# Performance work log

Measured on AMD Instinct MI355X. Metric: run time of the kernel, lower is better.

## Reference

```python
import jax, jax.numpy as jnp
import numpy as np

N = 8192        # nodes
IN_DIM = 512    # input feature dim
H = 8           # heads (hardcoded as 8 in original forward)
HID = 64        # out_feats per head
T = 10          # top-K threshold from settings['T']
OUT = 3         # classes
NEG = -9e15
NE_HALF = 131072  # half edges; graph made symmetric -> 262144 edges


def setup_inputs() -> dict:
    key = jax.random.key(0)
    ks = jax.random.split(key, 10)
    feat = jax.random.normal(ks[0], (N, IN_DIM), jnp.float32)

    def edges(k):
        k1, k2, k3 = jax.random.split(k, 3)
        u = jax.random.randint(k1, (NE_HALF,), 0, N, jnp.int32)
        v = jax.random.randint(k2, (NE_HALF,), 0, N, jnp.int32)
        src = jnp.concatenate([u, v])
        dst = jnp.concatenate([v, u])
        t = jax.random.uniform(k3, (NE_HALF,), jnp.float32) * 0.1  # TransM values
        trans = jnp.concatenate([t, t])
        return src, dst, trans

    src0, dst0, trans0 = edges(ks[1])
    src1, dst1, trans1 = edges(ks[2])
    fc_w0 = jax.random.normal(ks[3], (IN_DIM, H * HID), jnp.float32) * 0.05
    fc_w1 = jax.random.normal(ks[4], (IN_DIM, H * HID), jnp.float32) * 0.05
    sem_w1 = jax.random.normal(ks[5], (H * HID, 128), jnp.float32) * 0.05
    sem_b1 = jnp.zeros((128,), jnp.float32)
    sem_w2 = jax.random.normal(ks[6], (128,), jnp.float32) * 0.05
    lin_w = jax.random.normal(ks[7], (H * HID, OUT), jnp.float32) * 0.05
    lin_b = jnp.zeros((OUT,), jnp.float32)
    return dict(feat=feat, src0=src0, dst0=dst0, trans0=trans0,
                src1=src1, dst1=dst1, trans1=trans1,
                fc_w0=fc_w0, fc_w1=fc_w1, sem_w1=sem_w1, sem_b1=sem_b1,
                sem_w2=sem_w2, lin_w=lin_w, lin_b=lin_b)


def _rohe_conv(feat, src, dst, trans, fc_w):
    f = (feat @ fc_w).reshape(N, H, HID)               # (N,H,HID) projected feats
    # per-edge per-head dot products (same math as dense matmul + edge gather)
    e = jnp.einsum('ehd,ehd->eh', f[src], f[dst])      # (Ne,H)
    vals = trans * e.sum(-1)                           # (Ne,)  (e * e_trans).sum over heads
    # dense sparse->to_dense attn matrix, duplicates coalesced by sum
    A = jnp.zeros((N, N), f.dtype).at[src, dst].add(vals)
    kth = jax.lax.top_k(A, T)[0][:, -1]                # per-row T-th largest
    thr = jnp.maximum(kth, 0.0)                        # clamp(min=0)
    Am = jnp.where(A < thr[:, None], NEG, A)
    gathered = Am[dst, src]                            # == Am.T[src, dst]
    e = jnp.where((gathered < -100.0)[:, None], NEG, e)
    # edge softmax grouped by destination node, per head
    m = jax.ops.segment_max(e, dst, num_segments=N)
    ex = jnp.exp(e - m[dst])
    s = jax.ops.segment_sum(ex, dst, num_segments=N)
    a = ex / s[dst]                                    # (Ne,H)
    # u_mul_e + sum aggregation
    out = jax.ops.segment_sum(f[src] * a[:, :, None], dst, num_segments=N)
    return jax.nn.elu(out).reshape(N, H * HID)         # activation=F.elu, flatten(1)


def reference(feat, src0, dst0, trans0, src1, dst1, trans1,
              fc_w0, fc_w1, sem_w1, sem_b1, sem_w2, lin_w, lin_b):
    z0 = _rohe_conv(feat, src0, dst0, trans0, fc_w0)
    z1 = _rohe_conv(feat, src1, dst1, trans1, fc_w1)
    z = jnp.stack([z0, z1], axis=1)                    # (N, M=2, D)
    # SemanticAttention: project -> tanh -> score, mean over nodes, softmax over metapaths
    w = jnp.tanh(z @ sem_w1 + sem_b1) @ sem_w2         # (N, M)
    beta = jax.nn.softmax(w.mean(0))                   # (M,)
    h = (z * beta[None, :, None]).sum(1)               # (N, D)
    return h @ lin_w + lin_b                           # final nn.Linear
```

## Files before the change

kernel.cpp:

```cpp
#include <hip/hip_runtime.h>
#include <math.h>

#define NN      8192
#define DIM     512
#define NHEAD   8
#define HID     64
#define NE      262144
#define NE_HALF 131072
#define CMASK   (NE_HALF - 1)
#define TOPK    10
#define NEGV    -9e15f
#define MAXD    160
#define MAXC    64

typedef __attribute__((ext_vector_type(8))) short short8;
typedef __attribute__((ext_vector_type(4))) float f32x4;
typedef __attribute__((ext_vector_type(2))) int i32x2;
typedef __attribute__((ext_vector_type(4))) int i32x4;

__device__ __forceinline__ float bf2f(unsigned int h) {
    return __uint_as_float(h << 16);
}
__device__ __forceinline__ unsigned short f2bf(float x) {
    unsigned int u = __float_as_uint(x);
    unsigned int r = (u + 0x7fff + ((u >> 16) & 1)) >> 16;
    return (unsigned short)r;
}

__device__ __forceinline__ void scatter_body(int j, int c,
                                             const int* __restrict__ src0,
                                             const int* __restrict__ src1,
                                             const int* __restrict__ dst0,
                                             const int* __restrict__ dst1,
                                             const float* __restrict__ trans0,
                                             const float* __restrict__ trans1,
                                             int* curF, int* curC,
                                             i32x2* __restrict__ ed,
                                             i32x4* __restrict__ ce) {
    const int* s = c ? src1 : src0;
    const int* dt = c ? dst1 : dst0;
    int v = s[j];
    int dv = dt[j];
    int p = atomicAdd(&curF[c * NN + v], 1);
    if (p < MAXD) {
        i32x2 pk; pk.x = j; pk.y = dv;
        ed[(size_t)(c * NN + v) * MAXD + p] = pk;
    }
    if (j < NE_HALF) {
        const float* tr = c ? trans1 : trans0;
        int q = atomicAdd(&curC[c * NN + v], 1);
        if (q < MAXC) {
            i32x4 ck;
            ck.x = j; ck.y = dv; ck.z = __float_as_int(tr[j]); ck.w = 0;
            ce[(size_t)(c * NN + v) * MAXC + q] = ck;
        }
    }
}

__device__ __forceinline__ void gemm_body(int b,
                                          const unsigned short* __restrict__ Ah,
                                          const unsigned short* __restrict__ Al,
                                          const unsigned short* __restrict__ Bh,
                                          const unsigned short* __restrict__ Bl,
                                          float* __restrict__ Cf,
                                          unsigned short* __restrict__ Ch) {
    __shared__ unsigned short Ash[128][32];
    __shared__ unsigned short Asl[128][32];
    __shared__ unsigned short Bsh[64][32];
    __shared__ unsigned short Bsl[64][32];
    const int bm = (b >> 3) * 128;
    const int bn = (b & 7) * 64;
    const int tid = threadIdx.x;
    const int lane = tid & 63;
    const int wave = tid >> 6;
    const int wm = (wave >> 1) * 64, wn = (wave & 1) * 32;
    const int fr = lane & 15, fq = lane >> 4;
    const int sr = tid >> 2, sc = (tid & 3) * 8;
    f32x4 acc[4][2] = {};
    const unsigned short* Ahg = Ah + (size_t)(bm + sr) * DIM + sc;
    const unsigned short* Alg = Al + (size_t)(bm + sr) * DIM + sc;
    const unsigned short* Bhg = Bh + (size_t)(bn + sr) * DIM + sc;
    const unsigned short* Blg = Bl + (size_t)(bn + sr) * DIM + sc;
    for (int kb = 0; kb < DIM; kb += 32) {
        __syncthreads();
        __builtin_amdgcn_global_load_lds(
            (const __attribute__((address_space(1))) void*)(Ahg + kb),
            (__attribute__((address_space(3))) void*)(&Ash[sr][sc]), 16, 0, 0);
        __builtin_amdgcn_global_load_lds(
            (const __attribute__((address_space(1))) void*)(Ahg + (size_t)64 * DIM + kb),
            (__attribute__((address_space(3))) void*)(&Ash[sr + 64][sc]), 16, 0, 0);
        __builtin_amdgcn_global_load_lds(
            (const __attribute__((address_space(1))) void*)(Alg + kb),
            (__attribute__((address_space(3))) void*)(&Asl[sr][sc]), 16, 0, 0);
        __builtin_amdgcn_global_load_lds(
            (const __attribute__((address_space(1))) void*)(Alg + (size_t)64 * DIM + kb),
            (__attribute__((address_space(3))) void*)(&Asl[sr + 64][sc]), 16, 0, 0);
        if (sr < 64) {
            __builtin_amdgcn_global_load_lds(
                (const __attribute__((address_space(1))) void*)(Bhg + kb),
                (__attribute__((address_space(3))) void*)(&Bsh[sr][sc]), 16, 0, 0);
            __builtin_amdgcn_global_load_lds(
                (const __attribute__((address_space(1))) void*)(Blg + kb),
                (__attribute__((address_space(3))) void*)(&Bsl[sr][sc]), 16, 0, 0);
        }
        __syncthreads();
        short8 ah[4], al[4], bh[2], bl[2];
        #pragma unroll
        for (int i = 0; i < 4; i++) {
            ah[i] = *(const short8*)&Ash[wm + i * 16 + fr][fq * 8];
            al[i] = *(const short8*)&Asl[wm + i * 16 + fr][fq * 8];
        }
        #pragma unroll
        for (int i = 0; i < 2; i++) {
            bh[i] = *(const short8*)&Bsh[wn + i * 16 + fr][fq * 8];
            bl[i] = *(const short8*)&Bsl[wn + i * 16 + fr][fq * 8];
        }
        #pragma unroll
        for (int mi = 0; mi < 4; mi++)
            #pragma unroll
            for (int ni = 0; ni < 2; ni++) {
                acc[mi][ni] = __builtin_amdgcn_mfma_f32_16x16x32_bf16(ah[mi], bh[ni], acc[mi][ni], 0, 0, 0);
                acc[mi][ni] = __builtin_amdgcn_mfma_f32_16x16x32_bf16(al[mi], bh[ni], acc[mi][ni], 0, 0, 0);
                acc[mi][ni] = __builtin_amdgcn_mfma_f32_16x16x32_bf16(ah[mi], bl[ni], acc[mi][ni], 0, 0, 0);
            }
    }
    #pragma unroll
    for (int mi = 0; mi < 4; mi++)
        #pragma unroll
        for (int ni = 0; ni < 2; ni++)
            #pragma unroll
            for (int r = 0; r < 4; r++) {
                int row = bm + wm + mi * 16 + fq * 4 + r;
                int col = bn + wn + ni * 16 + fr;
                float v = acc[mi][ni][r];
                size_t off = (size_t)row * DIM + col;
                Cf[off] = v;
                Ch[off] = f2bf(v);
            }
}

__device__ __forceinline__ void edge_body(int n,
                                          const float* __restrict__ Cf,
                                          const int* __restrict__ cdeg,
                                          const i32x4* __restrict__ ce,
                                          float* __restrict__ e,
                                          float* __restrict__ vals) {
    int d = cdeg[n];
    if (d > MAXC) d = MAXC;
    if (d <= 0) return;
    int wave = threadIdx.x >> 6, lane = threadIdx.x & 63;
    const float4* pf = (const float4*)(Cf + (size_t)n * DIM);
    float4 f0 = pf[lane * 2], f1 = pf[lane * 2 + 1];
    const size_t s0 = (size_t)n * MAXC;
    for (int base = wave * 4; base < d; base += 16) {
        int em = d - base; if (em > 4) em = 4;
        i32x4 c[4];
        #pragma unroll
        for (int t = 0; t < 4; t++)
            c[t] = ce[s0 + base + (t < em ? t : 0)];
        float4 b0[4], b1[4];
        #pragma unroll
        for (int t = 0; t < 4; t++) {
            const float4* q = (const float4*)(Cf + (size_t)c[t].y * DIM);
            b0[t] = q[lane * 2];
            b1[t] = q[lane * 2 + 1];
        }
        float p[4];
        #pragma unroll
        for (int t = 0; t < 4; t++) {
            p[t]  = f0.x * b0[t].x + f0.y * b0[t].y + f0.z * b0[t].z + f0.w * b0[t].w;
            p[t] += f1.x * b1[t].x + f1.y * b1[t].y + f1.z * b1[t].z + f1.w * b1[t].w;
            p[t] += __shfl_xor(p[t], 1);
            p[t] += __shfl_xor(p[t], 2);
            p[t] += __shfl_xor(p[t], 4);
        }
        if ((lane & 7) == 0) {
            int h = lane >> 3;
            #pragma unroll
            for (int t = 0; t < 4; t++)
                if (t < em) e[(size_t)c[t].x * NHEAD + h] = p[t];
        }
        #pragma unroll
        for (int t = 0; t < 4; t++) {
            p[t] += __shfl_xor(p[t], 8);
            p[t] += __shfl_xor(p[t], 16);
            p[t] += __shfl_xor(p[t], 32);
        }
        if (lane == 0) {
            #pragma unroll
            for (int t = 0; t < 4; t++)
                if (t < em) vals[c[t].x] = __int_as_float(c[t].z) * p[t];
        }
    }
}

__device__ __forceinline__ void conv_body(int blk,
                                          const int* __restrict__ deg,
                                          const i32x2* __restrict__ ed,
                                          const float* __restrict__ e,
                                          const float* __restrict__ vals,
                                          const unsigned short* __restrict__ fb,
                                          unsigned short* __restrict__ zb) {
    const int tid = threadIdx.x;
    const int w = tid >> 6, lane = tid & 63;
    const int n = blk * 4 + w;
    int d = deg[n];
    if (d > MAXD) d = MAXD;
    const size_t s0 = (size_t)n * MAXD;
    __shared__ int   ssrc[4][MAXD];
    __shared__ int   sjc[4][MAXD];
    __shared__ float sval[4][MAXD];
    __shared__ float svc[4][MAXD];
    __shared__ unsigned char lead[4][MAXD];
    __shared__ short sk[4][MAXD];
    __shared__ float sms[4][2][NHEAD];
    __shared__ int nkept[4];

    for (int i = lane; i < d; i += 64) {
        i32x2 pk = ed[s0 + i];
        int jc = pk.x & CMASK;
        sjc[w][i] = jc;
        ssrc[w][i] = pk.y;
        sval[w][i] = vals[jc];
    }
    __syncthreads();
    for (int i = lane; i < d; i += 64) {
        int c = ssrc[w][i];
        float sum = 0.f;
        bool leader = true;
        for (int k = 0; k < d; k++) {
            if (ssrc[w][k] == c) {
                sum += sval[w][k];
                if (k < i) leader = false;
            }
        }
        svc[w][i] = sum;
        lead[w][i] = leader ? 1 : 0;
    }
    __syncthreads();
    {
        float v[3];
        #pragma unroll
        for (int s = 0; s < 3; s++) v[s] = -1.f;
        int cnt = 0;
        #pragma unroll
        for (int s = 0; s < 3; s++) {
            int i = lane + s * 64;
            if (i < d && lead[w][i] && svc[w][i] > 0.f) { v[s] = svc[w][i]; cnt++; }
        }
        cnt += __shfl_xor(cnt, 1);  cnt += __shfl_xor(cnt, 2);
        cnt += __shfl_xor(cnt, 4);  cnt += __shfl_xor(cnt, 8);
        cnt += __shfl_xor(cnt, 16); cnt += __shfl_xor(cnt, 32);
        float thr = 0.f;
        if (cnt >= TOPK) {
            unsigned long long key = 0;
            for (int t = 0; t < TOPK; t++) {
                unsigned int bb = 0; int bs = 0;
                #pragma unroll
                for (int s = 0; s < 3; s++) {
                    if (v[s] > 0.f) {
                        unsigned int b = __float_as_uint(v[s]);
                        if (b > bb) { bb = b; bs = s; }
                    }
                }
                key = ((unsigned long long)bb << 12) | (unsigned)(lane << 3) | (unsigned)bs;
                unsigned long long o;
                o = __shfl_xor(key, 1);  if (o > key) key = o;
                o = __shfl_xor(key, 2);  if (o > key) key = o;
                o = __shfl_xor(key, 4);  if (o > key) key = o;
                o = __shfl_xor(key, 8);  if (o > key) key = o;
                o = __shfl_xor(key, 16); if (o > key) key = o;
                o = __shfl_xor(key, 32); if (o > key) key = o;
                int owner = (int)((key >> 3) & 63);
                if (owner == lane) v[key & 7] = -1.f;
            }
            thr = __uint_as_float((unsigned int)(key >> 12));
        }
        int base = 0;
        for (int s = 0; s * 64 < d; s++) {
            int i = s * 64 + lane;
            bool kp = (i < d) && (svc[w][i] >= thr);
            unsigned long long m = __ballot(kp);
            int pos = base + __popcll(m & ((1ull << lane) - 1ull));
            if (kp) sk[w][pos] = (short)i;
            base += (int)__popcll(m);
        }
        if (base == 0) {
            for (int i = lane; i < d; i += 64) sk[w][i] = (short)i;
            if (lane == 0) nkept[w] = -d;
        } else if (lane == 0) nkept[w] = base;
    }
    __syncthreads();
    int nk = nkept[w];
    bool uni = nk < 0;
    int dk = uni ? -nk : nk;
    if (!uni) {
        int h = lane & 7, sub = lane >> 3;
        float m = -INFINITY;
        for (int k = sub; k < dk; k += 8)
            m = fmaxf(m, e[(size_t)sjc[w][sk[w][k]] * NHEAD + h]);
        m = fmaxf(m, __shfl_xor(m, 8));
        m = fmaxf(m, __shfl_xor(m, 16));
        m = fmaxf(m, __shfl_xor(m, 32));
        float s = 0.f;
        for (int k = sub; k < dk; k += 8)
            s += expf(e[(size_t)sjc[w][sk[w][k]] * NHEAD + h] - m);
        s += __shfl_xor(s, 8);
        s += __shfl_xor(s, 16);
        s += __shfl_xor(s, 32);
        if (sub == 0) { sms[w][0][h] = m; sms[w][1][h] = 1.0f / s; }
    }
    __syncthreads();
    int c0 = lane * 8;
    int h = lane >> 3;
    float a0 = 0.f, a1 = 0.f, a2 = 0.f, a3 = 0.f;
    float a4 = 0.f, a5 = 0.f, a6 = 0.f, a7 = 0.f;
    if (uni) {
        for (int k = 0; k < dk; k++) {
            int ii = sk[w][k];
            uint4 v = *(const uint4*)(fb + (size_t)ssrc[w][ii] * DIM + c0);
            a0 += bf2f(v.x & 0xffffu); a1 += bf2f(v.x >> 16);
            a2 += bf2f(v.y & 0xffffu); a3 += bf2f(v.y >> 16);
            a4 += bf2f(v.z & 0xffffu); a5 += bf2f(v.z >> 16);
            a6 += bf2f(v.w & 0xffffu); a7 += bf2f(v.w >> 16);
        }
        float invd = 1.0f / (float)d;
        a0 *= invd; a1 *= invd; a2 *= invd; a3 *= invd;
        a4 *= invd; a5 *= invd; a6 *= invd; a7 *= invd;
    } else {
        float m_h = sms[w][0][h], is_h = sms[w][1][h];
        for (int kb = 0; kb < dk; kb += 8) {
            int rem = dk - kb; if (rem > 8) rem = 8;
            float wv = 0.f;
            {
                int t = lane & 7;
                if (t < rem) {
                    int ii = sk[w][kb + t];
                    wv = expf(e[(size_t)sjc[w][ii] * NHEAD + h] - m_h) * is_h;
                }
            }
#define AGG(j) { \
            float wgt = __shfl(wv, (lane & 56) | (j)); \
            int ii2 = sk[w][kb + (j)]; \
            uint4 vv = *(const uint4*)(fb + (size_t)ssrc[w][ii2] * DIM + c0); \
            a0 += wgt * bf2f(vv.x & 0xffffu); a1 += wgt * bf2f(vv.x >> 16); \
            a2 += wgt * bf2f(vv.y & 0xffffu); a3 += wgt * bf2f(vv.y >> 16); \
            a4 += wgt * bf2f(vv.z & 0xffffu); a5 += wgt * bf2f(vv.z >> 16); \
            a6 += wgt * bf2f(vv.w & 0xffffu); a7 += wgt * bf2f(vv.w >> 16); }
            if (rem == 8) {
                AGG(0) AGG(1) AGG(2) AGG(3) AGG(4) AGG(5) AGG(6) AGG(7)
            } else {
                for (int j = 0; j < rem; j++) AGG(j)
            }
#undef AGG
        }
    }
    a0 = a0 > 0.f ? a0 : expf(a0) - 1.f;
    a1 = a1 > 0.f ? a1 : expf(a1) - 1.f;
    a2 = a2 > 0.f ? a2 : expf(a2) - 1.f;
    a3 = a3 > 0.f ? a3 : expf(a3) - 1.f;
    a4 = a4 > 0.f ? a4 : expf(a4) - 1.f;
    a5 = a5 > 0.f ? a5 : expf(a5) - 1.f;
    a6 = a6 > 0.f ? a6 : expf(a6) - 1.f;
    a7 = a7 > 0.f ? a7 : expf(a7) - 1.f;
    uint4 o;
    o.x = (unsigned)f2bf(a0) | ((unsigned)f2bf(a1) << 16);
    o.y = (unsigned)f2bf(a2) | ((unsigned)f2bf(a3) << 16);
    o.z = (unsigned)f2bf(a4) | ((unsigned)f2bf(a5) << 16);
    o.w = (unsigned)f2bf(a6) | ((unsigned)f2bf(a7) << 16);
    *(uint4*)(zb + (size_t)n * DIM + c0) = o;
}

__device__ __forceinline__ void lin_body(int blk,
                                         const unsigned short* __restrict__ zb,
                                         const float* __restrict__ lin_w,
                                         float* __restrict__ y) {
    int tid = threadIdx.x;
    int w = tid >> 6, lane = tid & 63;
    int n = blk * 4 + w;
    uint4 v = *(const uint4*)(zb + (size_t)n * DIM + lane * 8);
    float f[8];
    f[0] = bf2f(v.x & 0xffffu); f[1] = bf2f(v.x >> 16);
    f[2] = bf2f(v.y & 0xffffu); f[3] = bf2f(v.y >> 16);
    f[4] = bf2f(v.z & 0xffffu); f[5] = bf2f(v.z >> 16);
    f[6] = bf2f(v.w & 0xffffu); f[7] = bf2f(v.w >> 16);
    float lwv[24];
    #pragma unroll
    for (int q = 0; q < 6; q++)
        *(float4*)&lwv[q * 4] = ((const float4*)lin_w)[lane * 6 + q];
    float acc0 = 0.f, acc1 = 0.f, acc2 = 0.f;
    #pragma unroll
    for (int j = 0; j < 8; j++) {
        acc0 += f[j] * lwv[j * 3 + 0];
        acc1 += f[j] * lwv[j * 3 + 1];
        acc2 += f[j] * lwv[j * 3 + 2];
    }
    #pragma unroll
    for (int s = 1; s < 64; s <<= 1) {
        acc0 += __shfl_xor(acc0, s);
        acc1 += __shfl_xor(acc1, s);
        acc2 += __shfl_xor(acc2, s);
    }
    if (lane == 0) {
        y[n * 3 + 0] = acc0;
        y[n * 3 + 1] = acc1;
        y[n * 3 + 2] = acc2;
    }
}

__device__ __forceinline__ void sem_body(int bx,
                                         const unsigned short* __restrict__ Z,
                                         const unsigned short* __restrict__ W1hT,
                                         const unsigned short* __restrict__ W1lT,
                                         const float* __restrict__ b1,
                                         const float* __restrict__ w2,
                                         float* wsum_slot) {
    const int bm = bx * 64;
    const int tid = threadIdx.x;
    const int lane = tid & 63, wave = tid >> 6;
    const int fr = lane & 15, fq = lane >> 4;
    __shared__ unsigned short Zs[64][32];
    __shared__ unsigned short Wh[128][32];
    __shared__ unsigned short Wl[128][32];
    const int sr = tid >> 2, sc = (tid & 3) * 8;
    f32x4 acc[8] = {};
    const unsigned short* Zg  = Z    + (size_t)(bm + sr) * DIM + sc;
    const unsigned short* Whg = W1hT + (size_t)sr * DIM + sc;
    const unsigned short* Wlg = W1lT + (size_t)sr * DIM + sc;
    for (int kb = 0; kb < DIM; kb += 32) {
        __syncthreads();
        __builtin_amdgcn_global_load_lds(
            (const __attribute__((address_space(1))) void*)(Zg + kb),
            (__attribute__((address_space(3))) void*)(&Zs[sr][sc]), 16, 0, 0);
        __builtin_amdgcn_global_load_lds(
            (const __attribute__((address_space(1))) void*)(Whg + kb),
            (__attribute__((address_space(3))) void*)(&Wh[sr][sc]), 16, 0, 0);
        __builtin_amdgcn_global_load_lds(
            (const __attribute__((address_space(1))) void*)(Whg + (size_t)64 * DIM + kb),
            (__attribute__((address_space(3))) void*)(&Wh[sr + 64][sc]), 16, 0, 0);
        __builtin_amdgcn_global_load_lds(
            (const __attribute__((address_space(1))) void*)(Wlg + kb),
            (__attribute__((address_space(3))) void*)(&Wl[sr][sc]), 16, 0, 0);
        __builtin_amdgcn_global_load_lds(
            (const __attribute__((address_space(1))) void*)(Wlg + (size_t)64 * DIM + kb),
            (__attribute__((address_space(3))) void*)(&Wl[sr + 64][sc]), 16, 0, 0);
        __syncthreads();
        short8 af = *(const short8*)&Zs[wave * 16 + fr][fq * 8];
        #pragma unroll
        for (int ni = 0; ni < 8; ni++) {
            short8 bh = *(const short8*)&Wh[ni * 16 + fr][fq * 8];
            acc[ni] = __builtin_amdgcn_mfma_f32_16x16x32_bf16(af, bh, acc[ni], 0, 0, 0);
        }
        #pragma unroll
        for (int ni = 0; ni < 8; ni++) {
            short8 bl = *(const short8*)&Wl[ni * 16 + fr][fq * 8];
            acc[ni] = __builtin_amdgcn_mfma_f32_16x16x32_bf16(af, bl, acc[ni], 0, 0, 0);
        }
    }
    float local = 0.f;
    #pragma unroll
    for (int ni = 0; ni < 8; ni++) {
        int col = ni * 16 + fr;
        float bb = b1[col], ww = w2[col];
        #pragma unroll
        for (int r = 0; r < 4; r++)
            local += tanhf(acc[ni][r] + bb) * ww;
    }
    __shared__ float red[256];
    red[tid] = local;
    __syncthreads();
    for (int s = 128; s > 0; s >>= 1) {
        if (tid < s) red[tid] += red[tid + s];
        __syncthreads();
    }
    if (tid == 0) atomicAdd(wsum_slot, red[0]);
}

__device__ __forceinline__ void split_w_body(const float* __restrict__ W,
                                             unsigned short* __restrict__ Th,
                                             unsigned short* __restrict__ Tl,
                                             int n0, int k0, int ncols,
                                             float (*t)[33], int tid) {
    int tx = tid & 31, ty = tid >> 5;
    #pragma unroll
    for (int i = 0; i < 4; i++)
        t[ty + 8 * i][tx] = W[(size_t)(k0 + ty + 8 * i) * ncols + n0 + tx];
    __syncthreads();
    #pragma unroll
    for (int i = 0; i < 4; i++) {
        float x = t[tx][ty + 8 * i];
        unsigned short h = f2bf(x);
        size_t off = (size_t)(n0 + ty + 8 * i) * DIM + k0 + tx;
        Th[off] = h;
        Tl[off] = f2bf(x - bf2f(h));
    }
}

__global__ __launch_bounds__(256) void prep(const float* __restrict__ feat,
                                            const float* __restrict__ w1,
                                            const float* __restrict__ fcw0,
                                            const float* __restrict__ fcw1,
                                            unsigned short* __restrict__ fH,
                                            unsigned short* __restrict__ fL,
                                            unsigned short* __restrict__ W1hT,
                                            unsigned short* __restrict__ W1lT,
                                            unsigned short* __restrict__ BhT0,
                                            unsigned short* __restrict__ BlT0,
                                            unsigned short* __restrict__ BhT1,
                                            unsigned short* __restrict__ BlT1) {
    int b = blockIdx.x;
    __shared__ float t[32][33];
    if (b < 4096) {
        int i = b * 256 + threadIdx.x;
        float4 v = ((const float4*)feat)[i];
        unsigned short h0 = f2bf(v.x), h1 = f2bf(v.y), h2 = f2bf(v.z), h3 = f2bf(v.w);
        ushort4 hv; hv.x = h0; hv.y = h1; hv.z = h2; hv.w = h3;
        ushort4 lv;
        lv.x = f2bf(v.x - bf2f(h0));
        lv.y = f2bf(v.y - bf2f(h1));
        lv.z = f2bf(v.z - bf2f(h2));
        lv.w = f2bf(v.w - bf2f(h3));
        ((ushort4*)fH)[i] = hv;
        ((ushort4*)fL)[i] = lv;
    } else if (b < 4160) {
        int idx = b - 4096;
        split_w_body(w1, W1hT, W1lT, (idx & 3) * 32, (idx >> 2) * 32, 128, t, threadIdx.x);
    } else if (b < 4416) {
        int idx = b - 4160;
        split_w_body(fcw0, BhT0, BlT0, (idx & 15) * 32, (idx >> 4) * 32, DIM, t, threadIdx.x);
    } else {
        int idx = b - 4416;
        split_w_body(fcw1, BhT1, BlT1, (idx & 15) * 32, (idx >> 4) * 32, DIM, t, threadIdx.x);
    }
}

__global__ __launch_bounds__(256) void gemm_sc(const unsigned short* __restrict__ Ah,
                                               const unsigned short* __restrict__ Al,
                                               const unsigned short* __restrict__ Bh,
                                               const unsigned short* __restrict__ Bl,
                                               float* __restrict__ Cf,
                                               unsigned short* __restrict__ Ch,
                                               const int* __restrict__ src0,
                                               const int* __restrict__ src1,
                                               const int* __restrict__ dst0,
                                               const int* __restrict__ dst1,
                                               const float* __restrict__ trans0,
                                               const float* __restrict__ trans1,
                                               int* curF, int* curC,
                                               i32x2* __restrict__ ed,
                                               i32x4* __restrict__ ce) {
    int b = blockIdx.x;
    if (b < 512) {
        gemm_body(b, Ah, Al, Bh, Bl, Cf, Ch);
    } else {
        int sb = b - 512;
        int c = sb >> 10;
        int j = (sb & 1023) * 256 + threadIdx.x;
        scatter_body(j, c, src0, src1, dst0, dst1, trans0, trans1,
                     curF, curC, ed, ce);
    }
}

__global__ __launch_bounds__(256) void gemm_ed(const unsigned short* __restrict__ Ah,
                                               const unsigned short* __restrict__ Al,
                                               const unsigned short* __restrict__ Bh,
                                               const unsigned short* __restrict__ Bl,
                                               float* __restrict__ Cf1,
                                               unsigned short* __restrict__ Ch1,
                                               const float* __restrict__ Cf0,
                                               const int* __restrict__ cdeg0,
                                               const i32x4* __restrict__ ce0,
                                               float* __restrict__ e0,
                                               float* __restrict__ vals0) {
    int b = blockIdx.x;
    if (b < 512) {
        gemm_body(b, Ah, Al, Bh, Bl, Cf1, Ch1);
    } else {
        edge_body(b - 512, Cf0, cdeg0, ce0, e0, vals0);
    }
}

__global__ __launch_bounds__(256) void conv_ed(const int* __restrict__ degF0,
                                               const i32x2* __restrict__ ed0,
                                               const float* __restrict__ e0,
                                               const float* __restrict__ vals0,
                                               const unsigned short* __restrict__ Ch0,
                                               unsigned short* __restrict__ z0,
                                               const float* __restrict__ Cf1,
                                               const int* __restrict__ cdeg1,
                                               const i32x4* __restrict__ ce1,
                                               float* __restrict__ e1,
                                               float* __restrict__ vals1) {
    int b = blockIdx.x;
    if (b < 2048) {
        conv_body(b, degF0, ed0, e0, vals0, Ch0, z0);
    } else {
        edge_body(b - 2048, Cf1, cdeg1, ce1, e1, vals1);
    }
}

__global__ __launch_bounds__(256) void conv_lin(const int* __restrict__ degF1,
                                                const i32x2* __restrict__ ed1,
                                                const float* __restrict__ e1,
                                                const float* __restrict__ vals1,
                                                const unsigned short* __restrict__ Ch1,
                                                unsigned short* __restrict__ z1,
                                                const unsigned short* __restrict__ z0,
                                                const float* __restrict__ lin_w,
                                                float* __restrict__ y0) {
    int b = blockIdx.x;
    if (b < 2048) {
        conv_body(b, degF1, ed1, e1, vals1, Ch1, z1);
    } else {
        lin_body(b - 2048, z0, lin_w, y0);
    }
}

__global__ __launch_bounds__(256) void sem_lin(const unsigned short* __restrict__ z0,
                                               const unsigned short* __restrict__ z1,
                                               const unsigned short* __restrict__ W1hT,
                                               const unsigned short* __restrict__ W1lT,
                                               const float* __restrict__ b1,
                                               const float* __restrict__ w2,
                                               float* __restrict__ wsum,
                                               const float* __restrict__ lin_w,
                                               float* __restrict__ y1) {
    int b = blockIdx.x;
    if (b < 128) {
        sem_body(b, z0, W1hT, W1lT, b1, w2, &wsum[0]);
    } else if (b < 256) {
        sem_body(b - 128, z1, W1hT, W1lT, b1, w2, &wsum[1]);
    } else {
        lin_body(b - 256, z1, lin_w, y1);
    }
}

__global__ __launch_bounds__(256) void combine_out(const float* __restrict__ y0,
                                                   const float* __restrict__ y1,
                                                   const float* __restrict__ wsum,
                                                   const float* __restrict__ lin_b,
                                                   float* __restrict__ out) {
    int idx = blockIdx.x * 256 + threadIdx.x;
    float w0 = wsum[0] * (1.0f / NN), w1v = wsum[1] * (1.0f / NN);
    float mx = fmaxf(w0, w1v);
    float ea = expf(w0 - mx), eb = expf(w1v - mx);
    float beta0 = ea / (ea + eb), beta1 = eb / (ea + eb);
    int o = idx % 3;
    out[idx] = beta0 * y0[idx] + beta1 * y1[idx] + lin_b[o];
}

extern "C" void kernel_launch(void* const* d_in, const int* in_sizes, int n_in,
                              void* d_out, int out_size, void* d_ws, size_t ws_size,
                              hipStream_t stream) {
    const float* feat = (const float*)d_in[0];
    const int*   srcp[2]   = { (const int*)d_in[1], (const int*)d_in[4] };
    const int*   dstp[2]   = { (const int*)d_in[2], (const int*)d_in[5] };
    const float* transp[2] = { (const float*)d_in[3], (const float*)d_in[6] };
    const float* fcw[2]    = { (const float*)d_in[7], (const float*)d_in[8] };
    const float* sem_w1 = (const float*)d_in[9];
    const float* sem_b1 = (const float*)d_in[10];
    const float* sem_w2 = (const float*)d_in[11];
    const float* lin_w  = (const float*)d_in[12];
    const float* lin_b  = (const float*)d_in[13];
    float* out = (float*)d_out;

    char* ws = (char*)d_ws;
    const size_t MB = 1 << 20;
    const size_t KB = 1 << 10;
    if (ws_size < 128 * MB) return;
    float*          Cf0   = (float*)(ws);
    float*          Cf1   = (float*)(ws + 16 * MB);
    unsigned short* Ch0   = (unsigned short*)(ws + 32 * MB);
    unsigned short* Ch1   = (unsigned short*)(ws + 40 * MB);
    unsigned short* z0    = (unsigned short*)(ws + 48 * MB);
    unsigned short* z1    = (unsigned short*)(ws + 56 * MB);
    unsigned short* fH    = (unsigned short*)(ws + 64 * MB);
    unsigned short* fL    = (unsigned short*)(ws + 72 * MB);
    float*          e0    = (float*)(ws + 80 * MB);
    float*          e1    = (float*)(ws + 84 * MB);
    float*          vals0 = (float*)(ws + 88 * MB);
    float*          vals1 = (float*)(ws + 88 * MB + 512 * KB);
    i32x2*          ed    = (i32x2*)(ws + 89 * MB);
    i32x4*          ce    = (i32x4*)(ws + 109 * MB);
    unsigned short* BhT0  = (unsigned short*)(ws + 125 * MB);
    unsigned short* BlT0  = (unsigned short*)(ws + 125 * MB + 512 * KB);
    unsigned short* BhT1  = (unsigned short*)(ws + 126 * MB);
    unsigned short* BlT1  = (unsigned short*)(ws + 126 * MB + 512 * KB);
    unsigned short* W1hT  = (unsigned short*)(ws + 127 * MB);
    unsigned short* W1lT  = (unsigned short*)(ws + 127 * MB + 128 * KB);
    float*          y0    = (float*)(ws + 127 * MB + 256 * KB);
    float*          y1    = (float*)(ws + 127 * MB + 384 * KB);
    int*            cur   = (int*)  (ws + 127 * MB + 512 * KB);
    float*          wsum  = (float*)(ws + 127 * MB + 640 * KB);

    hipMemsetAsync(cur, 0, 4 * NN * sizeof(int) + 2 * sizeof(float), stream);
    prep<<<4672, 256, 0, stream>>>(feat, sem_w1, fcw[0], fcw[1],
                                   fH, fL, W1hT, W1lT, BhT0, BlT0, BhT1, BlT1);
    int* curF = cur;
    int* curC = cur + 2 * NN;
    gemm_sc<<<2560, 256, 0, stream>>>(fH, fL, BhT0, BlT0, Cf0, Ch0,
                                      srcp[0], srcp[1], dstp[0], dstp[1],
                                      transp[0], transp[1],
                                      curF, curC, ed, ce);
    gemm_ed<<<8704, 256, 0, stream>>>(fH, fL, BhT1, BlT1, Cf1, Ch1,
                                      Cf0, curC, ce, e0, vals0);
    conv_ed<<<10240, 256, 0, stream>>>(curF, ed, e0, vals0, Ch0, z0,
                                       Cf1, curC + NN, ce + (size_t)NN * MAXC,
                                       e1, vals1);
    conv_lin<<<4096, 256, 0, stream>>>(curF + NN, ed + (size_t)NN * MAXD,
                                       e1, vals1, Ch1, z1, z0, lin_w, y0);
    sem_lin<<<2304, 256, 0, stream>>>(z0, z1, W1hT, W1lT, sem_b1, sem_w2,
                                      wsum, lin_w, y1);
    combine_out<<<(NN * 3) / 256, 256, 0, stream>>>(y0, y1, wsum, lin_b, out);
}
```

Baseline: 322.4 us.

## Use per-wave barriers in conv and interleave heterogeneous blocks in fused kernels

Replaces block-wide __syncthreads in conv_body with a wave-local barrier (waitcnt plus wave_barrier), since each wave works on its own shared-memory slice, and broadcasts nkept via a shuffle. It also interleaves GEMM/conv blocks with scatter, edge and lin blocks by modular block-index mapping, so the heavy and light work types run concurrently across CUs instead of in contiguous ranges. This relies on the grid sizes matching the new ratios exactly, and on no cross-wave shared-memory dependence in conv_body.

```diff
diff --git a/kernel.cpp b/kernel.cpp
--- a/kernel.cpp
+++ b/kernel.cpp
@@ -25,6 +25,11 @@
     unsigned int u = __float_as_uint(x);
     unsigned int r = (u + 0x7fff + ((u >> 16) & 1)) >> 16;
     return (unsigned short)r;
+}
+
+__device__ __forceinline__ void wavebar() {
+    asm volatile("s_waitcnt lgkmcnt(0)" ::: "memory");
+    __builtin_amdgcn_wave_barrier();
 }
 
 __device__ __forceinline__ void scatter_body(int j, int c,
@@ -223,7 +228,7 @@
         ssrc[w][i] = pk.y;
         sval[w][i] = vals[jc];
     }
-    __syncthreads();
+    wavebar();
     for (int i = lane; i < d; i += 64) {
         int c = ssrc[w][i];
         float sum = 0.f;
@@ -237,7 +242,7 @@
         svc[w][i] = sum;
         lead[w][i] = leader ? 1 : 0;
     }
-    __syncthreads();
+    wavebar();
     {
         float v[3];
         #pragma unroll
@@ -290,8 +295,9 @@
             if (lane == 0) nkept[w] = -d;
         } else if (lane == 0) nkept[w] = base;
     }
-    __syncthreads();
+    wavebar();
     int nk = nkept[w];
+    nk = __shfl(nk, 0);
     bool uni = nk < 0;
     int dk = uni ? -nk : nk;
     if (!uni) {
@@ -310,7 +316,7 @@
         s += __shfl_xor(s, 32);
         if (sub == 0) { sms[w][0][h] = m; sms[w][1][h] = 1.0f / s; }
     }
-    __syncthreads();
+    wavebar();
     int c0 = lane * 8;
     int h = lane >> 3;
     float a0 = 0.f, a1 = 0.f, a2 = 0.f, a3 = 0.f;
@@ -550,10 +556,11 @@
                                                i32x2* __restrict__ ed,
                                                i32x4* __restrict__ ce) {
     int b = blockIdx.x;
-    if (b < 512) {
-        gemm_body(b, Ah, Al, Bh, Bl, Cf, Ch);
+    int g = b / 5;
+    if (b - g * 5 == 0) {
+        gemm_body(g, Ah, Al, Bh, Bl, Cf, Ch);
     } else {
-        int sb = b - 512;
+        int sb = b - g - 1;
         int c = sb >> 10;
         int j = (sb & 1023) * 256 + threadIdx.x;
         scatter_body(j, c, src0, src1, dst0, dst1, trans0, trans1,
@@ -573,10 +580,11 @@
                                                float* __restrict__ e0,
                                                float* __restrict__ vals0) {
     int b = blockIdx.x;
-    if (b < 512) {
-        gemm_body(b, Ah, Al, Bh, Bl, Cf1, Ch1);
+    int g = b / 17;
+    if (b - g * 17 == 0) {
+        gemm_body(g, Ah, Al, Bh, Bl, Cf1, Ch1);
     } else {
-        edge_body(b - 512, Cf0, cdeg0, ce0, e0, vals0);
+        edge_body(b - g - 1, Cf0, cdeg0, ce0, e0, vals0);
     }
 }
 
@@ -592,10 +600,11 @@
                                                float* __restrict__ e1,
                                                float* __restrict__ vals1) {
     int b = blockIdx.x;
-    if (b < 2048) {
-        conv_body(b, degF0, ed0, e0, vals0, Ch0, z0);
+    int g = b / 5;
+    if (b - g * 5 == 0) {
+        conv_body(g, degF0, ed0, e0, vals0, Ch0, z0);
     } else {
-        edge_body(b - 2048, Cf1, cdeg1, ce1, e1, vals1);
+        edge_body(b - g - 1, Cf1, cdeg1, ce1, e1, vals1);
     }
 }
 
@@ -609,10 +618,10 @@
                                                 const float* __restrict__ lin_w,
                                                 float* __restrict__ y0) {
     int b = blockIdx.x;
-    if (b < 2048) {
-        conv_body(b, degF1, ed1, e1, vals1, Ch1, z1);
+    if ((b & 1) == 0) {
+        conv_body(b >> 1, degF1, ed1, e1, vals1, Ch1, z1);
     } else {
-        lin_body(b - 2048, z0, lin_w, y0);
+        lin_body(b >> 1, z0, lin_w, y0);
     }
 }
 
```

New measurement: 367.5 us. 1.14x slower.
